# Kernel tuning notes

Hardware: AMD Instinct MI355X
Metric: run time of the kernel (lower is better)

The kernel has to match this reference:

```python
import jax, jax.numpy as jnp
import numpy as np

B, S, D, A = 16, 2048, 512, 512

def setup_inputs() -> dict:
    key = jax.random.key(0)
    ks = jax.random.split(key, 7)
    scale = 1.0 / np.sqrt(D)
    return {
        "query": jax.random.normal(ks[0], (B, S, D), dtype=jnp.float32),
        "key_": jax.random.normal(ks[1], (B, S, D), dtype=jnp.float32),
        "value": jax.random.normal(ks[2], (B, S, D), dtype=jnp.float32),
        "Wq": jax.random.normal(ks[3], (D, A), dtype=jnp.float32) * scale,
        "Wk": jax.random.normal(ks[4], (D, A), dtype=jnp.float32) * scale,
        "Wv": jax.random.normal(ks[5], (D, A), dtype=jnp.float32) * scale,
        "Ws": jax.random.normal(ks[6], (A, 1), dtype=jnp.float32) * (1.0 / np.sqrt(A)),
    }

def reference(query, key_, value, Wq, Wk, Wv, Ws):
    # Dense projections (no bias): [B,S,D] @ [D,A] -> [B,S,A]
    q = jnp.einsum("bsd,da->bsa", query, Wq)
    k = jnp.einsum("bsd,da->bsa", key_, Wk)
    v = jnp.einsum("bsd,da->bsa", value, Wv)
    # Additive (Bahdanau) scores: tanh(q+k) @ Ws -> [B,S]
    scores = jnp.einsum("bsa,a->bs", jnp.tanh(q + k), Ws[:, 0])
    attention_weights = jax.nn.softmax(scores, axis=1)[..., None]  # [B,S,1]
    context_vector = jnp.sum(attention_weights * v, axis=1)        # [B,A]
    return context_vector, attention_weights
```

## Files before the change

kernel.cpp:

```cpp
#include <hip/hip_runtime.h>
#include <stdint.h>

#define B_ 16
#define S_ 2048
#define D_ 512
#define A_ 512
#define M_TOT (B_ * S_)

typedef __attribute__((ext_vector_type(4))) float f32x4;
typedef __attribute__((ext_vector_type(8))) short bf16x8;

__device__ inline unsigned short f2bf(float f) {
  union { float f; unsigned int u; } c; c.f = f;
  unsigned int u = c.u;
  unsigned int r = (u + 0x7fffu + ((u >> 16) & 1u)) >> 16;
  return (unsigned short)r;
}

__device__ inline float fast_tanh(float x) {
  float e = __expf(2.0f * x);
  return 1.0f - 2.0f * __builtin_amdgcn_rcpf(e + 1.0f);
}

__device__ inline void gload_lds16(const void* g, void* l) {
  __builtin_amdgcn_global_load_lds((const __attribute__((address_space(1))) void*)g,
                                   (__attribute__((address_space(3))) void*)l, 16, 0, 0);
}

__global__ __launch_bounds__(256) void k0_pack_w(const float* __restrict__ Wq,
                                                 const float* __restrict__ Wk,
                                                 unsigned short* __restrict__ WT) {
  __shared__ unsigned short tile[64][65];
  int bid = blockIdx.x;
  int dt = bid & 15, at = bid >> 4;
  int d0 = dt * 64, a0 = at * 64;
  int t = threadIdx.x;
  int col = t & 63, rbase = t >> 6;
#pragma unroll
  for (int r8 = 0; r8 < 16; ++r8) {
    int row = r8 * 4 + rbase;
    int dcat = d0 + row;
    float f = (dcat < 512) ? Wq[(size_t)dcat * 512 + a0 + col]
                           : Wk[(size_t)(dcat - 512) * 512 + a0 + col];
    tile[row][col] = f2bf(f);
  }
  __syncthreads();
#pragma unroll
  for (int r8 = 0; r8 < 16; ++r8) {
    int arow = r8 * 4 + rbase;
    WT[(size_t)(a0 + arow) * 1024 + d0 + col] = tile[col][arow];
  }
}

__global__ __launch_bounds__(512, 2) void k1_scores(
    const float* __restrict__ Q, const float* __restrict__ K,
    const unsigned short* __restrict__ WT, const float* __restrict__ Wsv,
    float* __restrict__ score) {
  __shared__ unsigned short Al[128 * 64];
  __shared__ unsigned short Bl[512 * 64];
  __shared__ float sws[512];
  __shared__ float scw[8][128];

  const int t = threadIdx.x;
  const int lane = t & 63, w = t >> 6;
  const int frow = lane & 15;
  const int fsl = lane >> 4;
  const int row0 = (int)blockIdx.x * 128;

  sws[t] = Wsv[t];

  const int am = t >> 2;
  const int as0 = (t & 3) * 2;

  f32x4 acc[8][4];
#pragma unroll
  for (int m = 0; m < 8; ++m)
#pragma unroll
    for (int n = 0; n < 4; ++n) acc[m][n] = (f32x4){0.f, 0.f, 0.f, 0.f};

  auto stageA = [&](int kt) {
    int k0 = kt * 64;
    const float* src = (k0 < 512) ? Q : K;
    int kk = (k0 & 511) + as0 * 8;
    const float* ap = src + (size_t)(row0 + am) * 512 + kk;
    float4 f0 = *(const float4*)(ap + 0);
    float4 f1 = *(const float4*)(ap + 4);
    float4 f2 = *(const float4*)(ap + 8);
    float4 f3 = *(const float4*)(ap + 12);
    uint4 c0, c1;
    c0.x = f2bf(f0.x) | ((unsigned)f2bf(f0.y) << 16);
    c0.y = f2bf(f0.z) | ((unsigned)f2bf(f0.w) << 16);
    c0.z = f2bf(f1.x) | ((unsigned)f2bf(f1.y) << 16);
    c0.w = f2bf(f1.z) | ((unsigned)f2bf(f1.w) << 16);
    c1.x = f2bf(f2.x) | ((unsigned)f2bf(f2.y) << 16);
    c1.y = f2bf(f2.z) | ((unsigned)f2bf(f2.w) << 16);
    c1.z = f2bf(f3.x) | ((unsigned)f2bf(f3.y) << 16);
    c1.w = f2bf(f3.z) | ((unsigned)f2bf(f3.w) << 16);
    int d0 = (as0 ^ (am & 7)), d1 = ((as0 + 1) ^ (am & 7));
    *(uint4*)((char*)Al + am * 128 + d0 * 16) = c0;
    *(uint4*)((char*)Al + am * 128 + d1 * 16) = c1;
  };

  auto stageB = [&](int kt) {
    int k0 = kt * 64;
#pragma unroll
    for (int q = 0; q < 8; ++q) {
      int p = (w * 8 + q) * 64 + lane;
      int row = p >> 3;
      int sl = (p & 7) ^ (row & 7);
      const char* g = (const char*)WT + (size_t)row * 2048 + k0 * 2 + sl * 16;
      char* l = (char*)Bl + (size_t)(w * 8 + q) * 1024;
      gload_lds16(g, l);
    }
  };

  stageA(0);
  stageB(0);

  for (int kt = 0; kt < 16; ++kt) {
    __syncthreads();
    bf16x8 a0[8], b0[4];
#pragma unroll
    for (int m = 0; m < 8; ++m) {
      int row = m * 16 + frow;
      int sl = fsl ^ (row & 7);
      a0[m] = *(const bf16x8*)((const char*)Al + row * 128 + sl * 16);
    }
#pragma unroll
    for (int n = 0; n < 4; ++n) {
      int row = w * 64 + n * 16 + frow;
      int sl = fsl ^ (row & 7);
      b0[n] = *(const bf16x8*)((const char*)Bl + row * 128 + sl * 16);
    }
#pragma unroll
    for (int m = 0; m < 8; ++m)
#pragma unroll
      for (int n = 0; n < 4; ++n)
        acc[m][n] = __builtin_amdgcn_mfma_f32_16x16x32_bf16(a0[m], b0[n], acc[m][n], 0, 0, 0);
    bf16x8 a1[8], b1[4];
#pragma unroll
    for (int m = 0; m < 8; ++m) {
      int row = m * 16 + frow;
      int sl = (4 + fsl) ^ (row & 7);
      a1[m] = *(const bf16x8*)((const char*)Al + row * 128 + sl * 16);
    }
#pragma unroll
    for (int n = 0; n < 4; ++n) {
      int row = w * 64 + n * 16 + frow;
      int sl = (4 + fsl) ^ (row & 7);
      b1[n] = *(const bf16x8*)((const char*)Bl + row * 128 + sl * 16);
    }
    __syncthreads();
    if (kt < 15) { stageA(kt + 1); stageB(kt + 1); }
#pragma unroll
    for (int m = 0; m < 8; ++m)
#pragma unroll
      for (int n = 0; n < 4; ++n)
        acc[m][n] = __builtin_amdgcn_mfma_f32_16x16x32_bf16(a1[m], b1[n], acc[m][n], 0, 0, 0);
  }

#pragma unroll
  for (int m = 0; m < 8; ++m) {
#pragma unroll
    for (int ii = 0; ii < 4; ++ii) {
      float s = 0.f;
#pragma unroll
      for (int n = 0; n < 4; ++n)
        s += fast_tanh(acc[m][n][ii]) * sws[w * 64 + n * 16 + frow];
      s += __shfl_xor(s, 1);
      s += __shfl_xor(s, 2);
      s += __shfl_xor(s, 4);
      s += __shfl_xor(s, 8);
      if (frow == 0) scw[w][m * 16 + fsl * 4 + ii] = s;
    }
  }
  __syncthreads();
  if (t < 128) {
    float s = 0.f;
#pragma unroll
    for (int ww = 0; ww < 8; ++ww) s += scw[ww][t];
    score[row0 + t] = s;
  }
}

__global__ __launch_bounds__(256) void k2_softmax(const float* __restrict__ score,
                                                  float* __restrict__ outw) {
  int b = blockIdx.x, t = threadIdx.x;
  int lane = t & 63, wave = t >> 6;
  __shared__ float red[4], red2[4];
  float v[8];
  float mx = -1e30f;
#pragma unroll
  for (int e = 0; e < 8; ++e) {
    float p = score[(size_t)b * S_ + e * 256 + t];
    v[e] = p;
    mx = fmaxf(mx, p);
  }
  for (int off = 1; off < 64; off <<= 1) mx = fmaxf(mx, __shfl_xor(mx, off));
  if (lane == 0) red[wave] = mx;
  __syncthreads();
  mx = fmaxf(fmaxf(red[0], red[1]), fmaxf(red[2], red[3]));
  float sum = 0.f;
#pragma unroll
  for (int e = 0; e < 8; ++e) { v[e] = expf(v[e] - mx); sum += v[e]; }
  for (int off = 1; off < 64; off <<= 1) sum += __shfl_xor(sum, off);
  if (lane == 0) red2[wave] = sum;
  __syncthreads();
  sum = red2[0] + red2[1] + red2[2] + red2[3];
  float inv = 1.f / sum;
#pragma unroll
  for (int e = 0; e < 8; ++e)
    outw[(size_t)b * S_ + e * 256 + t] = v[e] * inv;
}

__global__ __launch_bounds__(256) void k3_vsum(const float* __restrict__ value,
                                               const float* __restrict__ w,
                                               float* __restrict__ upart) {
  int bid = blockIdx.x;
  int schunk = bid & 15, dchunk = (bid >> 4) & 1, b = bid >> 5;
  int t = threadIdx.x;
  __shared__ float wl[128];
  int s0 = schunk * 128;
  if (t < 128) wl[t] = w[(size_t)b * S_ + s0 + t];
  __syncthreads();
  const float* vp = value + ((size_t)b * S_ + s0) * 512 + dchunk * 256 + t;
  float a0 = 0.f, a1 = 0.f, a2 = 0.f, a3 = 0.f;
  for (int s = 0; s < 128; s += 4) {
    a0 += wl[s + 0] * vp[(size_t)(s + 0) * 512];
    a1 += wl[s + 1] * vp[(size_t)(s + 1) * 512];
    a2 += wl[s + 2] * vp[(size_t)(s + 2) * 512];
    a3 += wl[s + 3] * vp[(size_t)(s + 3) * 512];
  }
  upart[(size_t)(schunk * 16 + b) * 512 + dchunk * 256 + t] = (a0 + a1) + (a2 + a3);
}

__global__ __launch_bounds__(512) void k4_ctx(const float* __restrict__ upart,
                                              const float* __restrict__ Wv,
                                              float* __restrict__ out) {
  int b = blockIdx.x, t = threadIdx.x;
  __shared__ float ul[512];
  float u = 0.f;
#pragma unroll
  for (int c = 0; c < 16; ++c) u += upart[(size_t)(c * 16 + b) * 512 + t];
  ul[t] = u;
  __syncthreads();
  float acc = 0.f;
#pragma unroll 8
  for (int d = 0; d < 512; ++d) acc += ul[d] * Wv[(size_t)d * 512 + t];
  out[(size_t)b * 512 + t] = acc;
}

extern "C" void kernel_launch(void* const* d_in, const int* in_sizes, int n_in,
                              void* d_out, int out_size, void* d_ws, size_t ws_size,
                              hipStream_t stream) {
  const float* Q  = (const float*)d_in[0];
  const float* Kk = (const float*)d_in[1];
  const float* V  = (const float*)d_in[2];
  const float* Wq = (const float*)d_in[3];
  const float* Wk = (const float*)d_in[4];
  const float* Wv = (const float*)d_in[5];
  const float* Ws = (const float*)d_in[6];
  float* out = (float*)d_out;

  char* ws = (char*)d_ws;
  unsigned short* WT = (unsigned short*)ws;
  float* score = (float*)(ws + (1 << 20));
  float* upart = (float*)(ws + (1 << 20) + (512 << 10));

  float* outw = out + B_ * A_;

  k0_pack_w<<<dim3(128), dim3(256), 0, stream>>>(Wq, Wk, WT);
  k1_scores<<<dim3(256), dim3(512), 0, stream>>>(Q, Kk, WT, Ws, score);
  k2_softmax<<<dim3(16), dim3(256), 0, stream>>>(score, outw);
  k3_vsum<<<dim3(512), dim3(256), 0, stream>>>(V, outw, upart);
  k4_ctx<<<dim3(16), dim3(512), 0, stream>>>(upart, Wv, out);
}
```

Before: 103.3 us.

## Double-buffer score GEMM with smaller M tile and vectorize value reduction

The score GEMM kernel now works on 64-row tiles with a K step of 32 and double-buffered LDS. The next A tile is prefetched into registers two steps ahead, and stores and loads are overlapped with a single barrier per step. The grid doubles to 512 blocks and launch bounds now request 4 blocks per SM, so 256 CUs are filled and more memory traffic is in flight. The value-sum kernel switches to float4 loads with the S dimension split across waves and an LDS reduction. Tradeoffs are less reuse of B per block, since the weight tile is reloaded twice as often, and tighter register and LDS budgets.

```diff
diff --git a/kernel.cpp b/kernel.cpp
--- a/kernel.cpp
+++ b/kernel.cpp
@@ -52,115 +52,88 @@
   }
 }
 
-__global__ __launch_bounds__(512, 2) void k1_scores(
+__global__ __launch_bounds__(512, 4) void k1_scores(
     const float* __restrict__ Q, const float* __restrict__ K,
     const unsigned short* __restrict__ WT, const float* __restrict__ Wsv,
     float* __restrict__ score) {
-  __shared__ unsigned short Al[128 * 64];
-  __shared__ unsigned short Bl[512 * 64];
+  __shared__ unsigned short Al[2][64 * 32];
+  __shared__ unsigned short Bl[2][512 * 32];
   __shared__ float sws[512];
-  __shared__ float scw[8][128];
+  __shared__ float scw[8][64];
 
   const int t = threadIdx.x;
   const int lane = t & 63, w = t >> 6;
-  const int frow = lane & 15;
-  const int fsl = lane >> 4;
-  const int row0 = (int)blockIdx.x * 128;
+  const int frow = lane & 15, fsl = lane >> 4;
+  const int row0 = (int)blockIdx.x * 64;
 
   sws[t] = Wsv[t];
 
-  const int am = t >> 2;
-  const int as0 = (t & 3) * 2;
-
-  f32x4 acc[8][4];
-#pragma unroll
-  for (int m = 0; m < 8; ++m)
-#pragma unroll
-    for (int n = 0; n < 4; ++n) acc[m][n] = (f32x4){0.f, 0.f, 0.f, 0.f};
-
-  auto stageA = [&](int kt) {
-    int k0 = kt * 64;
-    const float* src = (k0 < 512) ? Q : K;
-    int kk = (k0 & 511) + as0 * 8;
-    const float* ap = src + (size_t)(row0 + am) * 512 + kk;
-    float4 f0 = *(const float4*)(ap + 0);
-    float4 f1 = *(const float4*)(ap + 4);
-    float4 f2 = *(const float4*)(ap + 8);
-    float4 f3 = *(const float4*)(ap + 12);
-    uint4 c0, c1;
-    c0.x = f2bf(f0.x) | ((unsigned)f2bf(f0.y) << 16);
-    c0.y = f2bf(f0.z) | ((unsigned)f2bf(f0.w) << 16);
-    c0.z = f2bf(f1.x) | ((unsigned)f2bf(f1.y) << 16);
-    c0.w = f2bf(f1.z) | ((unsigned)f2bf(f1.w) << 16);
-    c1.x = f2bf(f2.x) | ((unsigned)f2bf(f2.y) << 16);
-    c1.y = f2bf(f2.z) | ((unsigned)f2bf(f2.w) << 16);
-    c1.z = f2bf(f3.x) | ((unsigned)f2bf(f3.y) << 16);
-    c1.w = f2bf(f3.z) | ((unsigned)f2bf(f3.w) << 16);
-    int d0 = (as0 ^ (am & 7)), d1 = ((as0 + 1) ^ (am & 7));
-    *(uint4*)((char*)Al + am * 128 + d0 * 16) = c0;
-    *(uint4*)((char*)Al + am * 128 + d1 * 16) = c1;
+  const int ar = t >> 3, ak = (t & 7) * 4;
+  const int wchunk = (t & 7) >> 1;
+  const int wbyte = ar * 64 + ((wchunk ^ ((ar >> 1) & 3)) * 16) + (t & 1) * 8;
+
+  float4 areg[2];
+
+  auto issueA = [&](int kt, int j) {
+    int kcat = kt * 32;
+    const float* src = (kcat < 512) ? Q : K;
+    areg[j] = *(const float4*)(src + (size_t)(row0 + ar) * 512 + (kcat & 511) + ak);
   };
-
+  auto stageAW = [&](int j) {
+    float4 f = areg[j];
+    uint2 d;
+    d.x = f2bf(f.x) | ((unsigned)f2bf(f.y) << 16);
+    d.y = f2bf(f.z) | ((unsigned)f2bf(f.w) << 16);
+    *(uint2*)((char*)&Al[j][0] + wbyte) = d;
+  };
   auto stageB = [&](int kt) {
-    int k0 = kt * 64;
-#pragma unroll
-    for (int q = 0; q < 8; ++q) {
-      int p = (w * 8 + q) * 64 + lane;
-      int row = p >> 3;
-      int sl = (p & 7) ^ (row & 7);
-      const char* g = (const char*)WT + (size_t)row * 2048 + k0 * 2 + sl * 16;
-      char* l = (char*)Bl + (size_t)(w * 8 + q) * 1024;
+    int j = kt & 1;
+    int kb = kt * 64;
+#pragma unroll
+    for (int q = 0; q < 4; ++q) {
+      int p = (w * 4 + q) * 64 + lane;
+      int row = p >> 2;
+      int sl = (p & 3) ^ ((row >> 1) & 3);
+      const char* g = (const char*)WT + (size_t)row * 2048 + kb + sl * 16;
+      char* l = (char*)&Bl[j][0] + (size_t)(w * 4 + q) * 1024;
       gload_lds16(g, l);
     }
   };
 
-  stageA(0);
+  f32x4 acc[4][4];
+#pragma unroll
+  for (int m = 0; m < 4; ++m)
+#pragma unroll
+    for (int n = 0; n < 4; ++n) acc[m][n] = (f32x4){0.f, 0.f, 0.f, 0.f};
+
+  issueA(0, 0);
+  stageAW(0);
   stageB(0);
-
-  for (int kt = 0; kt < 16; ++kt) {
+  issueA(1, 1);
+
+#pragma unroll 2
+  for (int kt = 0; kt < 32; ++kt) {
+    const int cur = kt & 1;
     __syncthreads();
-    bf16x8 a0[8], b0[4];
-#pragma unroll
-    for (int m = 0; m < 8; ++m) {
-      int row = m * 16 + frow;
-      int sl = fsl ^ (row & 7);
-      a0[m] = *(const bf16x8*)((const char*)Al + row * 128 + sl * 16);
-    }
-#pragma unroll
-    for (int n = 0; n < 4; ++n) {
-      int row = w * 64 + n * 16 + frow;
-      int sl = fsl ^ (row & 7);
-      b0[n] = *(const bf16x8*)((const char*)Bl + row * 128 + sl * 16);
-    }
-#pragma unroll
-    for (int m = 0; m < 8; ++m)
+    if (kt + 2 < 32) issueA(kt + 2, cur);
+    if (kt + 1 < 32) { stageAW(cur ^ 1); stageB(kt + 1); }
+    bf16x8 af[4], bfr[4];
+    const int ch = (fsl ^ ((frow >> 1) & 3)) * 16;
+#pragma unroll
+    for (int m = 0; m < 4; ++m)
+      af[m] = *(const bf16x8*)((const char*)&Al[cur][0] + (m * 16 + frow) * 64 + ch);
+#pragma unroll
+    for (int n = 0; n < 4; ++n)
+      bfr[n] = *(const bf16x8*)((const char*)&Bl[cur][0] + (w * 64 + n * 16 + frow) * 64 + ch);
+#pragma unroll
+    for (int m = 0; m < 4; ++m)
 #pragma unroll
       for (int n = 0; n < 4; ++n)
-        acc[m][n] = __builtin_amdgcn_mfma_f32_16x16x32_bf16(a0[m], b0[n], acc[m][n], 0, 0, 0);
-    bf16x8 a1[8], b1[4];
-#pragma unroll
-    for (int m = 0; m < 8; ++m) {
-      int row = m * 16 + frow;
-      int sl = (4 + fsl) ^ (row & 7);
-      a1[m] = *(const bf16x8*)((const char*)Al + row * 128 + sl * 16);
-    }
-#pragma unroll
-    for (int n = 0; n < 4; ++n) {
-      int row = w * 64 + n * 16 + frow;
-      int sl = (4 + fsl) ^ (row & 7);
-      b1[n] = *(const bf16x8*)((const char*)Bl + row * 128 + sl * 16);
-    }
-    __syncthreads();
-    if (kt < 15) { stageA(kt + 1); stageB(kt + 1); }
-#pragma unroll
-    for (int m = 0; m < 8; ++m)
-#pragma unroll
-      for (int n = 0; n < 4; ++n)
-        acc[m][n] = __builtin_amdgcn_mfma_f32_16x16x32_bf16(a1[m], b1[n], acc[m][n], 0, 0, 0);
-  }
-
-#pragma unroll
-  for (int m = 0; m < 8; ++m) {
+        acc[m][n] = __builtin_amdgcn_mfma_f32_16x16x32_bf16(af[m], bfr[n], acc[m][n], 0, 0, 0);
+  }
+
+#pragma unroll
+  for (int m = 0; m < 4; ++m) {
 #pragma unroll
     for (int ii = 0; ii < 4; ++ii) {
       float s = 0.f;
@@ -175,7 +148,7 @@
     }
   }
   __syncthreads();
-  if (t < 128) {
+  if (t < 64) {
     float s = 0.f;
 #pragma unroll
     for (int ww = 0; ww < 8; ++ww) s += scw[ww][t];
@@ -217,21 +190,28 @@
                                                const float* __restrict__ w,
                                                float* __restrict__ upart) {
   int bid = blockIdx.x;
-  int schunk = bid & 15, dchunk = (bid >> 4) & 1, b = bid >> 5;
+  int dh = bid & 1, sc = (bid >> 1) & 15, b = bid >> 5;
   int t = threadIdx.x;
+  int dg = t & 63, sg = t >> 6;
   __shared__ float wl[128];
-  int s0 = schunk * 128;
+  __shared__ f32x4 red[4][64];
+  int s0 = sc * 128;
   if (t < 128) wl[t] = w[(size_t)b * S_ + s0 + t];
   __syncthreads();
-  const float* vp = value + ((size_t)b * S_ + s0) * 512 + dchunk * 256 + t;
-  float a0 = 0.f, a1 = 0.f, a2 = 0.f, a3 = 0.f;
-  for (int s = 0; s < 128; s += 4) {
-    a0 += wl[s + 0] * vp[(size_t)(s + 0) * 512];
-    a1 += wl[s + 1] * vp[(size_t)(s + 1) * 512];
-    a2 += wl[s + 2] * vp[(size_t)(s + 2) * 512];
-    a3 += wl[s + 3] * vp[(size_t)(s + 3) * 512];
-  }
-  upart[(size_t)(schunk * 16 + b) * 512 + dchunk * 256 + t] = (a0 + a1) + (a2 + a3);
+  const float* vp = value + ((size_t)b * S_ + s0) * 512 + dh * 256 + dg * 4;
+  f32x4 a = (f32x4){0.f, 0.f, 0.f, 0.f};
+  for (int s = sg; s < 128; s += 4) {
+    float4 v4 = *(const float4*)(vp + (size_t)s * 512);
+    float ws = wl[s];
+    a[0] += ws * v4.x; a[1] += ws * v4.y; a[2] += ws * v4.z; a[3] += ws * v4.w;
+  }
+  red[sg][dg] = a;
+  __syncthreads();
+  if (sg == 0) {
+    f32x4 r = red[0][dg] + red[1][dg] + red[2][dg] + red[3][dg];
+    float* dst = upart + (size_t)(sc * 16 + b) * 512 + dh * 256 + dg * 4;
+    dst[0] = r[0]; dst[1] = r[1]; dst[2] = r[2]; dst[3] = r[3];
+  }
 }
 
 __global__ __launch_bounds__(512) void k4_ctx(const float* __restrict__ upart,
@@ -270,7 +250,7 @@
   float* outw = out + B_ * A_;
 
   k0_pack_w<<<dim3(128), dim3(256), 0, stream>>>(Wq, Wk, WT);
-  k1_scores<<<dim3(256), dim3(512), 0, stream>>>(Q, Kk, WT, Ws, score);
+  k1_scores<<<dim3(512), dim3(512), 0, stream>>>(Q, Kk, WT, Ws, score);
   k2_softmax<<<dim3(16), dim3(256), 0, stream>>>(score, outw);
   k3_vsum<<<dim3(512), dim3(256), 0, stream>>>(V, outw, upart);
   k4_ctx<<<dim3(16), dim3(512), 0, stream>>>(upart, Wv, out);
```

After: 101.5 us. No clear change (-1.7%).
